# Kernel tuning notes

Measured on AMD Instinct MI355X. Metric: run time of the kernel, lower is better.

## Reference

```python
import jax, jax.numpy as jnp
import numpy as np

B, S, H, NH = 4, 1024, 2048, 32
HD = H // NH
EPS = 1e-5

def layer_norm(x, w, b):
    mu = jnp.mean(x, axis=-1, keepdims=True)
    var = jnp.mean(jnp.square(x - mu), axis=-1, keepdims=True)
    return (x - mu) * jax.lax.rsqrt(var + EPS) * w + b

def setup_inputs() -> dict:
    key = jax.random.key(0)
    ks = jax.random.split(key, 8)
    s = 0.02
    inp = {
        'hidden_states': jax.random.normal(ks[0], (B, S, H), jnp.float32),
        'mask': jnp.tril(jnp.ones((S, S), jnp.float32))[None, None],  # causal 0/1
        'ln1_w': jnp.ones((H,), jnp.float32), 'ln1_b': jnp.zeros((H,), jnp.float32),
        'w_qkv': s * jax.random.normal(ks[1], (H, 3 * H), jnp.float32),
        'b_qkv': jnp.zeros((3 * H,), jnp.float32),
        'w_dense': s * jax.random.normal(ks[2], (H, H), jnp.float32),
        'b_dense': jnp.zeros((H,), jnp.float32),
        'ln3_w': jnp.ones((H,), jnp.float32), 'ln3_b': jnp.zeros((H,), jnp.float32),
        'ln2_w': jnp.ones((H,), jnp.float32), 'ln2_b': jnp.zeros((H,), jnp.float32),
        'w_h4h': s * jax.random.normal(ks[3], (H, 4 * H), jnp.float32),
        'b_h4h': jnp.zeros((4 * H,), jnp.float32),
        'w_4hh': s * jax.random.normal(ks[4], (4 * H, H), jnp.float32),
        'b_4hh': jnp.zeros((H,), jnp.float32),
        'ln4_w': jnp.ones((H,), jnp.float32), 'ln4_b': jnp.zeros((H,), jnp.float32),
    }
    return inp

def _layer(hidden_states, mask, ln1_w, ln1_b, w_qkv, b_qkv, w_dense, b_dense,
           ln3_w, ln3_b, ln2_w, ln2_b, w_h4h, b_h4h, w_4hh, b_4hh, ln4_w, ln4_b):
    # --- input LN ---
    x1 = layer_norm(hidden_states, ln1_w, ln1_b)
    # --- self attention ---
    qkv = x1 @ w_qkv + b_qkv                              # [B,S,3H]
    q, k, v = jnp.split(qkv, 3, axis=-1)
    def heads(t):  # [B,S,H] -> [B,NH,S,HD]
        return t.reshape(B, S, NH, HD).transpose(0, 2, 1, 3)
    q, k, v = heads(q), heads(k), heads(v)
    scores = jnp.einsum('bnqd,bnkd->bnqk', q / jnp.sqrt(jnp.float32(HD)), k)
    scores = scores * mask - 10000.0 * (1.0 - mask)
    probs = jax.nn.softmax(scores, axis=-1)
    ctx = jnp.einsum('bnqk,bnkd->bnqd', probs, v)
    ctx = ctx.transpose(0, 2, 1, 3).reshape(B, S, H)
    attn_out = ctx @ w_dense + b_dense
    # sandwich LN on attention output
    attn_out = layer_norm(attn_out, ln3_w, ln3_b)
    ln_input = hidden_states + attn_out
    # --- MLP ---
    x2 = layer_norm(ln_input, ln2_w, ln2_b)
    inter = jax.nn.gelu(x2 @ w_h4h + b_h4h, approximate=True)
    mlp_out = inter @ w_4hh + b_4hh
    mlp_out = layer_norm(mlp_out, ln4_w, ln4_b)
    return ln_input + mlp_out

def reference(hidden_states, mask, ln1_w, ln1_b, w_qkv, b_qkv, w_dense, b_dense,
              ln3_w, ln3_b, ln2_w, ln2_b, w_h4h, b_h4h, w_4hh, b_4hh, ln4_w, ln4_b):
    return _layer(hidden_states, mask, ln1_w, ln1_b, w_qkv, b_qkv, w_dense, b_dense,
                  ln3_w, ln3_b, ln2_w, ln2_b, w_h4h, b_h4h, w_4hh, b_4hh, ln4_w, ln4_b)
```

## Files before the change

kernel.cpp:

```cpp
#include <hip/hip_runtime.h>
#include <cstdint>
#include <cstddef>

typedef __bf16 bf16_t;
typedef __bf16 bf16x8 __attribute__((ext_vector_type(8)));
typedef float f32x4 __attribute__((ext_vector_type(4)));

#define BB 4
#define SS 1024
#define HH 2048
#define NHH 32
#define HDD 64
#define MTOK 4096
#define QKVLD 6144

static constexpr size_t OFF_WQKV   = 0;
static constexpr size_t OFF_WDENSE = 25165824;
static constexpr size_t OFF_WH4H   = 33554432;
static constexpr size_t OFF_W4HH   = 67108864;
static constexpr size_t OFF_X1     = 100663296;
static constexpr size_t OFF_QKV    = 117440512;
static constexpr size_t OFF_ATTND2 = 150994944;
static constexpr size_t OFF_VT     = 167772160;
static constexpr size_t OFF_LNIN   = 184549376;
static constexpr size_t OFF_MLP    = 218103808;
static constexpr size_t OFF_MLP2   = 234881024;

__device__ __forceinline__ uint16_t f2bfu(float f) {
  union { float f; uint32_t u; } v; v.f = f;
  return (uint16_t)((v.u + 0x7FFFu + ((v.u >> 16) & 1u)) >> 16);
}
__device__ __forceinline__ bf16_t f2bf(float f) {
  union { uint16_t u; bf16_t b; } o; o.u = f2bfu(f);
  return o.b;
}
__device__ __forceinline__ float bfu2f(uint16_t u) {
  union { uint32_t u; float f; } v; v.u = ((uint32_t)u) << 16;
  return v.f;
}

__device__ __forceinline__ void g2l16(const void* g, void* l) {
  __builtin_amdgcn_global_load_lds(
      (const __attribute__((address_space(1))) void*)g,
      (__attribute__((address_space(3))) void*)l, 16, 0, 0);
}

__global__ void convert_all_kernel(const float* __restrict__ w0, bf16_t* __restrict__ o0,
                                   const float* __restrict__ w1, bf16_t* __restrict__ o1,
                                   const float* __restrict__ w2, bf16_t* __restrict__ o2,
                                   const float* __restrict__ w3, bf16_t* __restrict__ o3) {
  __shared__ float t[32][33];
  int id = blockIdx.x;
  const float* W; bf16_t* WT; int K, N, nt, idx;
  if (id < 12288)      { W = w0; WT = o0; K = 2048; N = 6144; nt = 192; idx = id; }
  else if (id < 16384) { W = w1; WT = o1; K = 2048; N = 2048; nt = 64;  idx = id - 12288; }
  else if (id < 32768) { W = w2; WT = o2; K = 2048; N = 8192; nt = 256; idx = id - 16384; }
  else                 { W = w3; WT = o3; K = 8192; N = 2048; nt = 64;  idx = id - 32768; }
  const int n0 = (idx % nt) * 32;
  const int k0 = (idx / nt) * 32;
  const int tx = threadIdx.x, ty = threadIdx.y;
#pragma unroll
  for (int j = 0; j < 4; ++j)
    t[ty + j * 8][tx] = W[(size_t)(k0 + ty + j * 8) * N + n0 + tx];
  __syncthreads();
#pragma unroll
  for (int j = 0; j < 4; ++j)
    WT[(size_t)(n0 + ty + j * 8) * K + k0 + tx] = f2bf(t[tx][ty + j * 8]);
}

__global__ void transpose_v_kernel(const bf16_t* __restrict__ qkv, bf16_t* __restrict__ vT) {
  __shared__ bf16_t t[32][33];
  const int s0 = blockIdx.x * 32;
  const int d0 = blockIdx.y * 32;
  const int bh = blockIdx.z;
  const int b = bh >> 5, h = bh & 31;
  const int tx = threadIdx.x, ty = threadIdx.y;
  const bf16_t* src = qkv + (size_t)b * SS * QKVLD + 2 * HH + h * HDD;
#pragma unroll
  for (int j = 0; j < 4; ++j)
    t[ty + j * 8][tx] = src[(size_t)(s0 + ty + j * 8) * QKVLD + d0 + tx];
  __syncthreads();
  bf16_t* dst = vT + (size_t)bh * HDD * SS;
#pragma unroll
  for (int j = 0; j < 4; ++j)
    dst[(size_t)(d0 + ty + j * 8) * SS + s0 + tx] = t[tx][ty + j * 8];
}

__device__ __forceinline__ void block_reduce2(float& s, float& ss) {
#pragma unroll
  for (int o = 32; o > 0; o >>= 1) {
    s += __shfl_down(s, o, 64);
    ss += __shfl_down(ss, o, 64);
  }
  __shared__ float red[8];
  const int wave = threadIdx.x >> 6;
  const int lane = threadIdx.x & 63;
  if (lane == 0) { red[wave] = s; red[4 + wave] = ss; }
  __syncthreads();
  s = red[0] + red[1] + red[2] + red[3];
  ss = red[4] + red[5] + red[6] + red[7];
  __syncthreads();
}

__device__ __forceinline__ void load8(const float* base, int tid, float* v) {
  float4 a = ((const float4*)base)[tid];
  float4 b = ((const float4*)base)[tid + 256];
  v[0] = a.x; v[1] = a.y; v[2] = a.z; v[3] = a.w;
  v[4] = b.x; v[5] = b.y; v[6] = b.z; v[7] = b.w;
}
__device__ __forceinline__ void load8bf(const bf16_t* base, int tid, float* v) {
  ushort4 a = ((const ushort4*)base)[tid];
  ushort4 b = ((const ushort4*)base)[tid + 256];
  v[0] = bfu2f(a.x); v[1] = bfu2f(a.y); v[2] = bfu2f(a.z); v[3] = bfu2f(a.w);
  v[4] = bfu2f(b.x); v[5] = bfu2f(b.y); v[6] = bfu2f(b.z); v[7] = bfu2f(b.w);
}
__device__ __forceinline__ void store8f(float* base, int tid, const float* v) {
  ((float4*)base)[tid] = make_float4(v[0], v[1], v[2], v[3]);
  ((float4*)base)[tid + 256] = make_float4(v[4], v[5], v[6], v[7]);
}
__device__ __forceinline__ void store8bf(bf16_t* base, int tid, const float* v) {
  ushort4 o0 = {f2bfu(v[0]), f2bfu(v[1]), f2bfu(v[2]), f2bfu(v[3])};
  ushort4 o1 = {f2bfu(v[4]), f2bfu(v[5]), f2bfu(v[6]), f2bfu(v[7])};
  ((ushort4*)base)[tid] = o0;
  ((ushort4*)base)[tid + 256] = o1;
}
__device__ __forceinline__ void row_stats(const float* v, float& mean, float& inv) {
  float s = 0.f, ss = 0.f;
#pragma unroll
  for (int i = 0; i < 8; ++i) { s += v[i]; ss += v[i] * v[i]; }
  block_reduce2(s, ss);
  mean = s * (1.0f / 2048.0f);
  float var = ss * (1.0f / 2048.0f) - mean * mean;
  inv = rsqrtf(var + 1e-5f);
}

__global__ __launch_bounds__(256) void ln1_kernel(const float* __restrict__ x,
                                                  const float* __restrict__ w,
                                                  const float* __restrict__ b,
                                                  bf16_t* __restrict__ out) {
  const int row = blockIdx.x, tid = threadIdx.x;
  float v[8], wv[8], bv[8], o[8];
  load8(x + (size_t)row * HH, tid, v);
  float mean, inv;
  row_stats(v, mean, inv);
  load8(w, tid, wv);
  load8(b, tid, bv);
#pragma unroll
  for (int i = 0; i < 8; ++i) o[i] = (v[i] - mean) * inv * wv[i] + bv[i];
  store8bf(out + (size_t)row * HH, tid, o);
}

__global__ __launch_bounds__(256) void fuse_mid_kernel(
    const bf16_t* __restrict__ ad, const bf16_t* __restrict__ ad2,
    const float* __restrict__ hid,
    const float* __restrict__ w3, const float* __restrict__ b3,
    const float* __restrict__ w2, const float* __restrict__ b2,
    float* __restrict__ lnin, bf16_t* __restrict__ x2) {
  const int row = blockIdx.x, tid = threadIdx.x;
  float a[8], a2[8], h[8], wv[8], bv[8], l[8], o[8];
  load8bf(ad + (size_t)row * HH, tid, a);
  load8bf(ad2 + (size_t)row * HH, tid, a2);
#pragma unroll
  for (int i = 0; i < 8; ++i) a[i] += a2[i];
  float mean3, inv3;
  row_stats(a, mean3, inv3);
  load8(hid + (size_t)row * HH, tid, h);
  load8(w3, tid, wv);
  load8(b3, tid, bv);
#pragma unroll
  for (int i = 0; i < 8; ++i) l[i] = h[i] + (a[i] - mean3) * inv3 * wv[i] + bv[i];
  store8f(lnin + (size_t)row * HH, tid, l);
  float mean2, inv2;
  row_stats(l, mean2, inv2);
  load8(w2, tid, wv);
  load8(b2, tid, bv);
#pragma unroll
  for (int i = 0; i < 8; ++i) o[i] = (l[i] - mean2) * inv2 * wv[i] + bv[i];
  store8bf(x2 + (size_t)row * HH, tid, o);
}

__global__ __launch_bounds__(256) void fuse_out_kernel(
    const bf16_t* __restrict__ mlp, const bf16_t* __restrict__ mlp2,
    const float* __restrict__ lnin,
    const float* __restrict__ w4, const float* __restrict__ b4,
    float* __restrict__ out) {
  const int row = blockIdx.x, tid = threadIdx.x;
  float m[8], m2[8], l[8], wv[8], bv[8], o[8];
  load8bf(mlp + (size_t)row * HH, tid, m);
  load8bf(mlp2 + (size_t)row * HH, tid, m2);
#pragma unroll
  for (int i = 0; i < 8; ++i) m[i] += m2[i];
  float mean4, inv4;
  row_stats(m, mean4, inv4);
  load8(lnin + (size_t)row * HH, tid, l);
  load8(w4, tid, wv);
  load8(b4, tid, bv);
#pragma unroll
  for (int i = 0; i < 8; ++i) o[i] = l[i] + (m[i] - mean4) * inv4 * wv[i] + bv[i];
  store8f(out + (size_t)row * HH, tid, o);
}

#define MFMA16(a, b, cc) __builtin_amdgcn_mfma_f32_16x16x32_bf16(a, b, cc, 0, 0, 0)

#define STAGE(ISB, BUF, HALF, KT) do {                                              \
    const char* _s = ((ISB) ? bS : aS) + (size_t)(HALF) * h128 + (size_t)(KT) * 128; \
    char* _d = lds + ((ISB) ? 65536 : 0) + (BUF) * 32768 + (HALF) * 16384 +         \
               wave * 1024;                                                         \
    g2l16(_s, _d);                                                                  \
    g2l16(_s + h64, _d + 8192);                                                     \
  } while (0)

#define LDA(BUF, MQ)                                                                \
  _Pragma("unroll") for (int mf = 0; mf < 4; ++mf) {                                \
    const char* _p = aRd + (BUF) * 32768 + (MQ) * 8192 + mf * 2048;                 \
    aR[mf * 2]     = *(const bf16x8*)(_p + colK0);                                  \
    aR[mf * 2 + 1] = *(const bf16x8*)(_p + colK1);                                  \
  }

#define LDB(BR, BUF, NQ)                                                            \
  _Pragma("unroll") for (int nf = 0; nf < 2; ++nf) {                                \
    const char* _p = bRd + (BUF) * 32768 + (NQ) * 4096 + nf * 2048;                 \
    BR[nf * 2]     = *(const bf16x8*)(_p + colK0);                                  \
    BR[nf * 2 + 1] = *(const bf16x8*)(_p + colK1);                                  \
  }

#define MMA(MQ, NQ, BR)                                                             \
  _Pragma("unroll") for (int mf = 0; mf < 4; ++mf)                                  \
  _Pragma("unroll") for (int nf = 0; nf < 2; ++nf)                                  \
  _Pragma("unroll") for (int ks = 0; ks < 2; ++ks)                                  \
    acc[(MQ) * 4 + mf][(NQ) * 2 + nf] =                                             \
        MFMA16(aR[mf * 2 + ks], BR[nf * 2 + ks], acc[(MQ) * 4 + mf][(NQ) * 2 + nf]);

#define PH_BEGIN()                                                                  \
  __builtin_amdgcn_s_barrier();                                                     \
  __builtin_amdgcn_s_setprio(1);

#define PH_MID()                                                                    \
  __builtin_amdgcn_s_setprio(0);

#define PH_END()                                                                    \
  __builtin_amdgcn_s_barrier();

template <int EPI, int SPLITK>
__global__ __launch_bounds__(512, 2) void gemm256(
    const bf16_t* __restrict__ A, const bf16_t* __restrict__ BT,
    const float* __restrict__ bias, void* __restrict__ out0, void* __restrict__ out1,
    const int M, const int N, const int Keff, const int ldK) {
  __shared__ alignas(16) char lds[131072];
  const int tid = threadIdx.x;
  const int wave = tid >> 6, lane = tid & 63;
  const int wm = wave >> 2, wn = wave & 3;
  const int c = lane & 15, g = lane >> 4;

  const int nwg = gridDim.x;
  int bid = (blockIdx.x & 7) * (nwg >> 3) + (blockIdx.x >> 3);
  const int nm = M >> 8;
  int slice = 0;
  if (SPLITK == 2) {
    const int per = nm * (N >> 8);
    slice = bid >= per;
    bid -= slice * per;
  }
  const int mt = bid % nm, nt = bid / nm;

  const size_t ldb = (size_t)ldK * 2;
  const size_t h64 = (size_t)64 * ldb;
  const size_t h128 = 2 * h64;
  const char* aPan = (const char*)A + (size_t)(mt * 256) * ldb + (size_t)(slice * Keff) * 2;
  const char* bPan = (const char*)BT + (size_t)(nt * 256) * ldb + (size_t)(slice * Keff) * 2;

  const int srow = tid >> 3;
  const int scb = ((tid & 7) << 4) ^ ((srow & 7) << 4);
  const char* aS = aPan + (size_t)srow * ldb + scb;
  const char* bS = bPan + (size_t)srow * ldb + scb;

  const int x4 = (c & 7) << 4;
  const int colK0 = (g * 16) ^ x4;
  const int colK1 = (64 + g * 16) ^ x4;
  const char* aRd = lds + wm * 16384 + c * 128;
  const char* bRd = lds + 65536 + (wn >> 1) * 16384 + ((wn & 1) * 64 + c) * 128;

  f32x4 acc[8][4] = {};
  bf16x8 aR[8], b0R[4], b1R[4];

  const int NITER = Keff >> 7;
  const int NT2 = NITER * 2;

  STAGE(1, 0, 0, 0); STAGE(1, 0, 1, 0); STAGE(0, 0, 0, 0); STAGE(0, 0, 1, 0);
  STAGE(1, 1, 0, 1); STAGE(1, 1, 1, 1);
  asm volatile("s_waitcnt vmcnt(4)" ::: "memory");
  __builtin_amdgcn_s_barrier();
  LDA(0, 0);
  LDB(b0R, 0, 0);

  for (int it = 0; it < NITER; ++it) {
    const int ktb = 2 * it + 1;
    int kt2 = 2 * it + 2; if (kt2 >= NT2) kt2 = 0;
    int kt3 = 2 * it + 3; if (kt3 >= NT2) kt3 = 0;
    STAGE(0, 1, 0, ktb);
    PH_BEGIN(); MMA(0, 0, b0R); PH_MID();
    LDB(b1R, 0, 1);
    PH_END();
    STAGE(0, 1, 1, ktb);
    PH_BEGIN(); MMA(0, 1, b1R); PH_MID();
    LDA(0, 1);
    PH_END();
    STAGE(1, 0, 0, kt2);
    PH_BEGIN(); MMA(1, 1, b1R); PH_MID();
    PH_END();
    STAGE(1, 0, 1, kt2);
    asm volatile("s_waitcnt vmcnt(4)" ::: "memory");
    PH_BEGIN(); MMA(1, 0, b0R); PH_MID();
    LDA(1, 0); LDB(b0R, 1, 0);
    PH_END();
    STAGE(0, 0, 0, kt2);
    PH_BEGIN(); MMA(0, 0, b0R); PH_MID();
    LDB(b1R, 1, 1);
    PH_END();
    STAGE(0, 0, 1, kt2);
    PH_BEGIN(); MMA(0, 1, b1R); PH_MID();
    LDA(1, 1);
    PH_END();
    STAGE(1, 1, 0, kt3);
    PH_BEGIN(); MMA(1, 1, b1R); PH_MID();
    PH_END();
    STAGE(1, 1, 1, kt3);
    asm volatile("s_waitcnt vmcnt(4)" ::: "memory");
    PH_BEGIN(); MMA(1, 0, b0R); PH_MID();
    LDA(0, 0); LDB(b0R, 0, 0);
    PH_END();
  }

  const int rowb = mt * 256 + wm * 128 + g * 4;
  const int colb = nt * 256 + wn * 64 + c;
  if constexpr (EPI == 0) {
    bf16_t* o = (bf16_t*)(slice ? out1 : out0);
    float bvv[4];
#pragma unroll
    for (int nf = 0; nf < 4; ++nf) bvv[nf] = (slice == 0) ? bias[colb + nf * 16] : 0.0f;
#pragma unroll
    for (int mf = 0; mf < 8; ++mf) {
      const int r = rowb + mf * 16;
#pragma unroll
      for (int e = 0; e < 4; ++e) {
        bf16_t* orow = o + (size_t)(r + e) * N + colb;
#pragma unroll
        for (int nf = 0; nf < 4; ++nf)
          orow[nf * 16] = f2bf(acc[mf][nf][e] + bvv[nf]);
      }
    }
  } else if constexpr (EPI == 1) {
    bf16_t* o = (bf16_t*)out0;
    float bvv[4];
#pragma unroll
    for (int nf = 0; nf < 4; ++nf) bvv[nf] = bias[colb + nf * 16];
#pragma unroll
    for (int mf = 0; mf < 8; ++mf) {
      const int r = rowb + mf * 16;
#pragma unroll
      for (int e = 0; e < 4; ++e) {
        bf16_t* orow = o + (size_t)(r + e) * N + colb;
#pragma unroll
        for (int nf = 0; nf < 4; ++nf)
          orow[nf * 16] = f2bf(acc[mf][nf][e] + bvv[nf]);
      }
    }
  } else {
    bf16_t* o = (bf16_t*)out0;
    float bvv[4];
#pragma unroll
    for (int nf = 0; nf < 4; ++nf) bvv[nf] = bias[colb + nf * 16];
#pragma unroll
    for (int mf = 0; mf < 8; ++mf) {
      const int r = rowb + mf * 16;
#pragma unroll
      for (int e = 0; e < 4; ++e) {
        bf16_t* orow = o + (size_t)(r + e) * N + colb;
#pragma unroll
        for (int nf = 0; nf < 4; ++nf) {
          float u = acc[mf][nf][e] + bvv[nf];
          float cc2 = 0.7978845608f * (u + 0.044715f * u * u * u);
          float ex = __expf(2.0f * cc2);
          float th = 1.0f - 2.0f / (ex + 1.0f);
          orow[nf * 16] = f2bf(0.5f * u * (1.0f + th));
        }
      }
    }
  }
}

__global__ __launch_bounds__(512) void attn_kernel(
    const bf16_t* __restrict__ qkv, const bf16_t* __restrict__ vT,
    bf16_t* __restrict__ ctx) {
  __shared__ alignas(16) char Ksm[8192];
  __shared__ alignas(16) char Vsm[8192];
  __shared__ alignas(16) char Psm[16384];

  const int id = blockIdx.x;
  const int qt = 7 - (id >> 7);
  const int bh = id & 127;
  const int b = bh >> 5, h = bh & 31;
  const int tid = threadIdx.x;
  const int wave = tid >> 6;
  const int lane = tid & 63;
  const int q0 = qt * 128;
  const int q0w = q0 + wave * 16;
  const int c = lane & 15;
  const int g = lane >> 4;

  const bf16_t* qb = qkv + ((size_t)b * SS + q0w) * QKVLD + h * HDD;
  const bf16x8 qa0 = *(const bf16x8*)(qb + (size_t)c * QKVLD + g * 8);
  const bf16x8 qa1 = *(const bf16x8*)(qb + (size_t)c * QKVLD + 32 + g * 8);

  f32x4 o[4] = {};
  float mrow[4], lrow[4];
#pragma unroll
  for (int e = 0; e < 4; ++e) { mrow[e] = -1e30f; lrow[e] = 0.0f; }

  const int sr = tid >> 3;
  const int sgb = ((tid & 7) * 16) ^ ((sr & 7) << 4);
  const char* kgb = (const char*)(qkv + (size_t)b * SS * QKVLD + HH + h * HDD);
  const char* vgb = (const char*)(vT + (size_t)bh * HDD * SS);
  char* kdst = Ksm + wave * 1024;
  char* vdst = Vsm + wave * 1024;
  char* Pw = Psm + wave * 2048;

  const int ntiles = (q0 + 128) >> 6;

  for (int t = 0; t < ntiles; ++t) {
    const int kb = t * 64;
    g2l16(kgb + (size_t)(kb + sr) * (QKVLD * 2) + sgb, kdst);
    g2l16(vgb + (size_t)sr * 2048 + (size_t)kb * 2 + sgb, vdst);
    __syncthreads();

    if (kb < q0w + 16) {
      f32x4 s[4] = {};
#pragma unroll
      for (int sub = 0; sub < 4; ++sub) {
        const int n = sub * 16 + c;
        const int x = (n & 7) << 4;
        bf16x8 kf0 = *(const bf16x8*)(Ksm + n * 128 + ((g * 16) ^ x));
        bf16x8 kf1 = *(const bf16x8*)(Ksm + n * 128 + ((64 + g * 16) ^ x));
        s[sub] = MFMA16(qa0, kf0, s[sub]);
        s[sub] = MFMA16(qa1, kf1, s[sub]);
      }
      const bool diag = (kb + 63 > q0w);
      float pv[4][4];
#pragma unroll
      for (int sub = 0; sub < 4; ++sub)
#pragma unroll
        for (int e = 0; e < 4; ++e) {
          float sv = s[sub][e] * 0.125f;
          if (diag && (kb + sub * 16 + c > q0w + g * 4 + e)) sv = -10000.0f;
          pv[sub][e] = sv;
        }
      float scale[4];
#pragma unroll
      for (int e = 0; e < 4; ++e) {
        float mx = fmaxf(fmaxf(pv[0][e], pv[1][e]), fmaxf(pv[2][e], pv[3][e]));
        mx = fmaxf(mx, __shfl_xor(mx, 1, 64));
        mx = fmaxf(mx, __shfl_xor(mx, 2, 64));
        mx = fmaxf(mx, __shfl_xor(mx, 4, 64));
        mx = fmaxf(mx, __shfl_xor(mx, 8, 64));
        const float mnew = fmaxf(mrow[e], mx);
        scale[e] = __expf(mrow[e] - mnew);
        mrow[e] = mnew;
      }
#pragma unroll
      for (int e = 0; e < 4; ++e) {
        const int row = g * 4 + e;
        const int xr = (row & 7) << 4;
        float sum = 0.0f;
#pragma unroll
        for (int sub = 0; sub < 4; ++sub) {
          float p = __expf(pv[sub][e] - mrow[e]);
          sum += p;
          const int cb = (sub * 16 + c) * 2;
          *(bf16_t*)(Pw + row * 128 + (cb ^ xr)) = f2bf(p);
        }
        sum += __shfl_xor(sum, 1, 64);
        sum += __shfl_xor(sum, 2, 64);
        sum += __shfl_xor(sum, 4, 64);
        sum += __shfl_xor(sum, 8, 64);
        lrow[e] = lrow[e] * scale[e] + sum;
      }
#pragma unroll
      for (int d = 0; d < 4; ++d)
#pragma unroll
        for (int e = 0; e < 4; ++e) o[d][e] *= scale[e];
      const int xa = (c & 7) << 4;
      bf16x8 pa0 = *(const bf16x8*)(Pw + c * 128 + ((g * 16) ^ xa));
      bf16x8 pa1 = *(const bf16x8*)(Pw + c * 128 + ((64 + g * 16) ^ xa));
#pragma unroll
      for (int d = 0; d < 4; ++d) {
        const int n = d * 16 + c;
        const int xv = (n & 7) << 4;
        bf16x8 vf0 = *(const bf16x8*)(Vsm + n * 128 + ((g * 16) ^ xv));
        bf16x8 vf1 = *(const bf16x8*)(Vsm + n * 128 + ((64 + g * 16) ^ xv));
        o[d] = MFMA16(pa0, vf0, o[d]);
        o[d] = MFMA16(pa1, vf1, o[d]);
      }
    }
    __syncthreads();
  }

#pragma unroll
  for (int e = 0; e < 4; ++e) {
    const int qrow = q0w + g * 4 + e;
    const float inv = 1.0f / lrow[e];
#pragma unroll
    for (int d = 0; d < 4; ++d)
      ctx[((size_t)b * SS + qrow) * HH + h * 64 + d * 16 + c] = f2bf(o[d][e] * inv);
  }
}

extern "C" void kernel_launch(void* const* d_in, const int* in_sizes, int n_in,
                              void* d_out, int out_size, void* d_ws, size_t ws_size,
                              hipStream_t stream) {
  const float* hidden = (const float*)d_in[0];
  const float* ln1w = (const float*)d_in[2];
  const float* ln1b = (const float*)d_in[3];
  const float* wqkv = (const float*)d_in[4];
  const float* bqkv = (const float*)d_in[5];
  const float* wdense = (const float*)d_in[6];
  const float* bdense = (const float*)d_in[7];
  const float* ln3w = (const float*)d_in[8];
  const float* ln3b = (const float*)d_in[9];
  const float* ln2w = (const float*)d_in[10];
  const float* ln2b = (const float*)d_in[11];
  const float* wh4h = (const float*)d_in[12];
  const float* bh4h = (const float*)d_in[13];
  const float* w4hh = (const float*)d_in[14];
  const float* b4hh = (const float*)d_in[15];
  const float* ln4w = (const float*)d_in[16];
  const float* ln4b = (const float*)d_in[17];

  char* ws = (char*)d_ws;
  bf16_t* wqkvT = (bf16_t*)(ws + OFF_WQKV);
  bf16_t* wdenseT = (bf16_t*)(ws + OFF_WDENSE);
  bf16_t* wh4hT = (bf16_t*)(ws + OFF_WH4H);
  bf16_t* w4hhT = (bf16_t*)(ws + OFF_W4HH);
  bf16_t* x1 = (bf16_t*)(ws + OFF_X1);
  bf16_t* qkv = (bf16_t*)(ws + OFF_QKV);
  bf16_t* vT = (bf16_t*)(ws + OFF_VT);
  bf16_t* ctx = (bf16_t*)(ws + OFF_X1);
  bf16_t* attnd = (bf16_t*)(ws + OFF_QKV);
  bf16_t* attnd2 = (bf16_t*)(ws + OFF_ATTND2);
  float* lnin = (float*)(ws + OFF_LNIN);
  bf16_t* x2 = (bf16_t*)(ws + OFF_X1);
  bf16_t* inter = (bf16_t*)(ws + OFF_QKV);
  bf16_t* mlp = (bf16_t*)(ws + OFF_MLP);
  bf16_t* mlp2 = (bf16_t*)(ws + OFF_MLP2);

  dim3 tb(32, 8);
  convert_all_kernel<<<dim3(49152), tb, 0, stream>>>(wqkv, wqkvT, wdense, wdenseT,
                                                     wh4h, wh4hT, w4hh, w4hhT);

  ln1_kernel<<<MTOK, 256, 0, stream>>>(hidden, ln1w, ln1b, x1);

  gemm256<1, 1><<<dim3((6144 / 256) * (4096 / 256)), 512, 0, stream>>>(
      x1, wqkvT, bqkv, (void*)qkv, nullptr, MTOK, 6144, 2048, 2048);

  transpose_v_kernel<<<dim3(SS / 32, HDD / 32, BB * NHH), tb, 0, stream>>>(qkv, vT);

  attn_kernel<<<dim3(1024), 512, 0, stream>>>(qkv, vT, ctx);

  gemm256<0, 2><<<dim3((2048 / 256) * (4096 / 256) * 2), 512, 0, stream>>>(
      ctx, wdenseT, bdense, (void*)attnd, (void*)attnd2, MTOK, 2048, 1024, 2048);

  fuse_mid_kernel<<<MTOK, 256, 0, stream>>>(attnd, attnd2, hidden, ln3w, ln3b, ln2w, ln2b, lnin, x2);

  gemm256<2, 1><<<dim3((8192 / 256) * (4096 / 256)), 512, 0, stream>>>(
      x2, wh4hT, bh4h, (void*)inter, nullptr, MTOK, 8192, 2048, 2048);

  gemm256<0, 2><<<dim3((2048 / 256) * (4096 / 256) * 2), 512, 0, stream>>>(
      inter, w4hhT, b4hh, (void*)mlp, (void*)mlp2, MTOK, 2048, 4096, 8192);

  fuse_out_kernel<<<MTOK, 256, 0, stream>>>(mlp, mlp2, lnin, ln4w, ln4b, (float*)d_out);
}
```

Before: 592.7 us.

## Double-buffer attention K/V tiles, fuse LN1 into weight convert, store lnin as bf16

The attention kernel now double-buffers its K and V shared-memory tiles, prefetching the next tile while the current one is computed, which removes the load-then-sync stall at the top of each iteration. The LN1 kernel is merged into the weight-conversion launch as extra blocks, saving one kernel launch. The residual lnin buffer is stored as bf16 instead of fp32, halving its traffic at the cost of precision in the final residual add. The prefetch appears to lack a barrier before the buffer is overwritten (only one __syncthreads per iteration), which may introduce a race.

```diff
diff --git a/kernel.cpp b/kernel.cpp
--- a/kernel.cpp
+++ b/kernel.cpp
@@ -45,12 +45,77 @@
       (__attribute__((address_space(3))) void*)l, 16, 0, 0);
 }
 
-__global__ void convert_all_kernel(const float* __restrict__ w0, bf16_t* __restrict__ o0,
+__device__ __forceinline__ void block_reduce2(int tid, float& s, float& ss) {
+#pragma unroll
+  for (int o = 32; o > 0; o >>= 1) {
+    s += __shfl_down(s, o, 64);
+    ss += __shfl_down(ss, o, 64);
+  }
+  __shared__ float red[8];
+  const int wave = tid >> 6;
+  const int lane = tid & 63;
+  if (lane == 0) { red[wave] = s; red[4 + wave] = ss; }
+  __syncthreads();
+  s = red[0] + red[1] + red[2] + red[3];
+  ss = red[4] + red[5] + red[6] + red[7];
+  __syncthreads();
+}
+
+__device__ __forceinline__ void load8(const float* base, int tid, float* v) {
+  float4 a = ((const float4*)base)[tid];
+  float4 b = ((const float4*)base)[tid + 256];
+  v[0] = a.x; v[1] = a.y; v[2] = a.z; v[3] = a.w;
+  v[4] = b.x; v[5] = b.y; v[6] = b.z; v[7] = b.w;
+}
+__device__ __forceinline__ void load8bf(const bf16_t* base, int tid, float* v) {
+  ushort4 a = ((const ushort4*)base)[tid];
+  ushort4 b = ((const ushort4*)base)[tid + 256];
+  v[0] = bfu2f(a.x); v[1] = bfu2f(a.y); v[2] = bfu2f(a.z); v[3] = bfu2f(a.w);
+  v[4] = bfu2f(b.x); v[5] = bfu2f(b.y); v[6] = bfu2f(b.z); v[7] = bfu2f(b.w);
+}
+__device__ __forceinline__ void store8f(float* base, int tid, const float* v) {
+  ((float4*)base)[tid] = make_float4(v[0], v[1], v[2], v[3]);
+  ((float4*)base)[tid + 256] = make_float4(v[4], v[5], v[6], v[7]);
+}
+__device__ __forceinline__ void store8bf(bf16_t* base, int tid, const float* v) {
+  ushort4 o0 = {f2bfu(v[0]), f2bfu(v[1]), f2bfu(v[2]), f2bfu(v[3])};
+  ushort4 o1 = {f2bfu(v[4]), f2bfu(v[5]), f2bfu(v[6]), f2bfu(v[7])};
+  ((ushort4*)base)[tid] = o0;
+  ((ushort4*)base)[tid + 256] = o1;
+}
+__device__ __forceinline__ void row_stats(int tid, const float* v, float& mean, float& inv) {
+  float s = 0.f, ss = 0.f;
+#pragma unroll
+  for (int i = 0; i < 8; ++i) { s += v[i]; ss += v[i] * v[i]; }
+  block_reduce2(tid, s, ss);
+  mean = s * (1.0f / 2048.0f);
+  float var = ss * (1.0f / 2048.0f) - mean * mean;
+  inv = rsqrtf(var + 1e-5f);
+}
+
+__global__ void convert_ln1_kernel(const float* __restrict__ w0, bf16_t* __restrict__ o0,
                                    const float* __restrict__ w1, bf16_t* __restrict__ o1,
                                    const float* __restrict__ w2, bf16_t* __restrict__ o2,
-                                   const float* __restrict__ w3, bf16_t* __restrict__ o3) {
+                                   const float* __restrict__ w3, bf16_t* __restrict__ o3,
+                                   const float* __restrict__ hid,
+                                   const float* __restrict__ ln1w, const float* __restrict__ ln1b,
+                                   bf16_t* __restrict__ x1) {
+  const int id = blockIdx.x;
+  const int tx = threadIdx.x & 31, ty = threadIdx.x >> 5;
+  if (id >= 49152) {
+    const int row = id - 49152, tid = threadIdx.x;
+    float v[8], wv[8], bv[8], o[8];
+    load8(hid + (size_t)row * HH, tid, v);
+    float mean, inv;
+    row_stats(tid, v, mean, inv);
+    load8(ln1w, tid, wv);
+    load8(ln1b, tid, bv);
+#pragma unroll
+    for (int i = 0; i < 8; ++i) o[i] = (v[i] - mean) * inv * wv[i] + bv[i];
+    store8bf(x1 + (size_t)row * HH, tid, o);
+    return;
+  }
   __shared__ float t[32][33];
-  int id = blockIdx.x;
   const float* W; bf16_t* WT; int K, N, nt, idx;
   if (id < 12288)      { W = w0; WT = o0; K = 2048; N = 6144; nt = 192; idx = id; }
   else if (id < 16384) { W = w1; WT = o1; K = 2048; N = 2048; nt = 64;  idx = id - 12288; }
@@ -58,7 +123,6 @@
   else                 { W = w3; WT = o3; K = 8192; N = 2048; nt = 64;  idx = id - 32768; }
   const int n0 = (idx % nt) * 32;
   const int k0 = (idx / nt) * 32;
-  const int tx = threadIdx.x, ty = threadIdx.y;
 #pragma unroll
   for (int j = 0; j < 4; ++j)
     t[ty + j * 8][tx] = W[(size_t)(k0 + ty + j * 8) * N + n0 + tx];
@@ -86,76 +150,12 @@
     dst[(size_t)(d0 + ty + j * 8) * SS + s0 + tx] = t[tx][ty + j * 8];
 }
 
-__device__ __forceinline__ void block_reduce2(float& s, float& ss) {
-#pragma unroll
-  for (int o = 32; o > 0; o >>= 1) {
-    s += __shfl_down(s, o, 64);
-    ss += __shfl_down(ss, o, 64);
-  }
-  __shared__ float red[8];
-  const int wave = threadIdx.x >> 6;
-  const int lane = threadIdx.x & 63;
-  if (lane == 0) { red[wave] = s; red[4 + wave] = ss; }
-  __syncthreads();
-  s = red[0] + red[1] + red[2] + red[3];
-  ss = red[4] + red[5] + red[6] + red[7];
-  __syncthreads();
-}
-
-__device__ __forceinline__ void load8(const float* base, int tid, float* v) {
-  float4 a = ((const float4*)base)[tid];
-  float4 b = ((const float4*)base)[tid + 256];
-  v[0] = a.x; v[1] = a.y; v[2] = a.z; v[3] = a.w;
-  v[4] = b.x; v[5] = b.y; v[6] = b.z; v[7] = b.w;
-}
-__device__ __forceinline__ void load8bf(const bf16_t* base, int tid, float* v) {
-  ushort4 a = ((const ushort4*)base)[tid];
-  ushort4 b = ((const ushort4*)base)[tid + 256];
-  v[0] = bfu2f(a.x); v[1] = bfu2f(a.y); v[2] = bfu2f(a.z); v[3] = bfu2f(a.w);
-  v[4] = bfu2f(b.x); v[5] = bfu2f(b.y); v[6] = bfu2f(b.z); v[7] = bfu2f(b.w);
-}
-__device__ __forceinline__ void store8f(float* base, int tid, const float* v) {
-  ((float4*)base)[tid] = make_float4(v[0], v[1], v[2], v[3]);
-  ((float4*)base)[tid + 256] = make_float4(v[4], v[5], v[6], v[7]);
-}
-__device__ __forceinline__ void store8bf(bf16_t* base, int tid, const float* v) {
-  ushort4 o0 = {f2bfu(v[0]), f2bfu(v[1]), f2bfu(v[2]), f2bfu(v[3])};
-  ushort4 o1 = {f2bfu(v[4]), f2bfu(v[5]), f2bfu(v[6]), f2bfu(v[7])};
-  ((ushort4*)base)[tid] = o0;
-  ((ushort4*)base)[tid + 256] = o1;
-}
-__device__ __forceinline__ void row_stats(const float* v, float& mean, float& inv) {
-  float s = 0.f, ss = 0.f;
-#pragma unroll
-  for (int i = 0; i < 8; ++i) { s += v[i]; ss += v[i] * v[i]; }
-  block_reduce2(s, ss);
-  mean = s * (1.0f / 2048.0f);
-  float var = ss * (1.0f / 2048.0f) - mean * mean;
-  inv = rsqrtf(var + 1e-5f);
-}
-
-__global__ __launch_bounds__(256) void ln1_kernel(const float* __restrict__ x,
-                                                  const float* __restrict__ w,
-                                                  const float* __restrict__ b,
-                                                  bf16_t* __restrict__ out) {
-  const int row = blockIdx.x, tid = threadIdx.x;
-  float v[8], wv[8], bv[8], o[8];
-  load8(x + (size_t)row * HH, tid, v);
-  float mean, inv;
-  row_stats(v, mean, inv);
-  load8(w, tid, wv);
-  load8(b, tid, bv);
-#pragma unroll
-  for (int i = 0; i < 8; ++i) o[i] = (v[i] - mean) * inv * wv[i] + bv[i];
-  store8bf(out + (size_t)row * HH, tid, o);
-}
-
 __global__ __launch_bounds__(256) void fuse_mid_kernel(
     const bf16_t* __restrict__ ad, const bf16_t* __restrict__ ad2,
     const float* __restrict__ hid,
     const float* __restrict__ w3, const float* __restrict__ b3,
     const float* __restrict__ w2, const float* __restrict__ b2,
-    float* __restrict__ lnin, bf16_t* __restrict__ x2) {
+    bf16_t* __restrict__ lnin, bf16_t* __restrict__ x2) {
   const int row = blockIdx.x, tid = threadIdx.x;
   float a[8], a2[8], h[8], wv[8], bv[8], l[8], o[8];
   load8bf(ad + (size_t)row * HH, tid, a);
@@ -163,15 +163,15 @@
 #pragma unroll
   for (int i = 0; i < 8; ++i) a[i] += a2[i];
   float mean3, inv3;
-  row_stats(a, mean3, inv3);
+  row_stats(tid, a, mean3, inv3);
   load8(hid + (size_t)row * HH, tid, h);
   load8(w3, tid, wv);
   load8(b3, tid, bv);
 #pragma unroll
   for (int i = 0; i < 8; ++i) l[i] = h[i] + (a[i] - mean3) * inv3 * wv[i] + bv[i];
-  store8f(lnin + (size_t)row * HH, tid, l);
+  store8bf(lnin + (size_t)row * HH, tid, l);
   float mean2, inv2;
-  row_stats(l, mean2, inv2);
+  row_stats(tid, l, mean2, inv2);
   load8(w2, tid, wv);
   load8(b2, tid, bv);
 #pragma unroll
@@ -181,7 +181,7 @@
 
 __global__ __launch_bounds__(256) void fuse_out_kernel(
     const bf16_t* __restrict__ mlp, const bf16_t* __restrict__ mlp2,
-    const float* __restrict__ lnin,
+    const bf16_t* __restrict__ lnin,
     const float* __restrict__ w4, const float* __restrict__ b4,
     float* __restrict__ out) {
   const int row = blockIdx.x, tid = threadIdx.x;
@@ -191,8 +191,8 @@
 #pragma unroll
   for (int i = 0; i < 8; ++i) m[i] += m2[i];
   float mean4, inv4;
-  row_stats(m, mean4, inv4);
-  load8(lnin + (size_t)row * HH, tid, l);
+  row_stats(tid, m, mean4, inv4);
+  load8bf(lnin + (size_t)row * HH, tid, l);
   load8(w4, tid, wv);
   load8(b4, tid, bv);
 #pragma unroll
@@ -392,8 +392,8 @@
 __global__ __launch_bounds__(512) void attn_kernel(
     const bf16_t* __restrict__ qkv, const bf16_t* __restrict__ vT,
     bf16_t* __restrict__ ctx) {
-  __shared__ alignas(16) char Ksm[8192];
-  __shared__ alignas(16) char Vsm[8192];
+  __shared__ alignas(16) char Ksm[2][8192];
+  __shared__ alignas(16) char Vsm[2][8192];
   __shared__ alignas(16) char Psm[16384];
 
   const int id = blockIdx.x;
@@ -421,17 +421,24 @@
   const int sgb = ((tid & 7) * 16) ^ ((sr & 7) << 4);
   const char* kgb = (const char*)(qkv + (size_t)b * SS * QKVLD + HH + h * HDD);
   const char* vgb = (const char*)(vT + (size_t)bh * HDD * SS);
-  char* kdst = Ksm + wave * 1024;
-  char* vdst = Vsm + wave * 1024;
   char* Pw = Psm + wave * 2048;
 
   const int ntiles = (q0 + 128) >> 6;
+
+  {
+    g2l16(kgb + (size_t)sr * (QKVLD * 2) + sgb, Ksm[0] + wave * 1024);
+    g2l16(vgb + (size_t)sr * 2048 + sgb, Vsm[0] + wave * 1024);
+  }
+  __syncthreads();
 
   for (int t = 0; t < ntiles; ++t) {
     const int kb = t * 64;
-    g2l16(kgb + (size_t)(kb + sr) * (QKVLD * 2) + sgb, kdst);
-    g2l16(vgb + (size_t)sr * 2048 + (size_t)kb * 2 + sgb, vdst);
-    __syncthreads();
+    const int cur = t & 1;
+    if (t + 1 < ntiles) {
+      const int kb1 = kb + 64;
+      g2l16(kgb + (size_t)(kb1 + sr) * (QKVLD * 2) + sgb, Ksm[cur ^ 1] + wave * 1024);
+      g2l16(vgb + (size_t)sr * 2048 + (size_t)kb1 * 2 + sgb, Vsm[cur ^ 1] + wave * 1024);
+    }
 
     if (kb < q0w + 16) {
       f32x4 s[4] = {};
@@ -439,8 +446,8 @@
       for (int sub = 0; sub < 4; ++sub) {
         const int n = sub * 16 + c;
         const int x = (n & 7) << 4;
-        bf16x8 kf0 = *(const bf16x8*)(Ksm + n * 128 + ((g * 16) ^ x));
-        bf16x8 kf1 = *(const bf16x8*)(Ksm + n * 128 + ((64 + g * 16) ^ x));
+        bf16x8 kf0 = *(const bf16x8*)(Ksm[cur] + n * 128 + ((g * 16) ^ x));
+        bf16x8 kf1 = *(const bf16x8*)(Ksm[cur] + n * 128 + ((64 + g * 16) ^ x));
         s[sub] = MFMA16(qa0, kf0, s[sub]);
         s[sub] = MFMA16(qa1, kf1, s[sub]);
       }
@@ -495,8 +502,8 @@
       for (int d = 0; d < 4; ++d) {
         const int n = d * 16 + c;
         const int xv = (n & 7) << 4;
-        bf16x8 vf0 = *(const bf16x8*)(Vsm + n * 128 + ((g * 16) ^ xv));
-        bf16x8 vf1 = *(const bf16x8*)(Vsm + n * 128 + ((64 + g * 16) ^ xv));
+        bf16x8 vf0 = *(const bf16x8*)(Vsm[cur] + n * 128 + ((g * 16) ^ xv));
+        bf16x8 vf1 = *(const bf16x8*)(Vsm[cur] + n * 128 + ((64 + g * 16) ^ xv));
         o[d] = MFMA16(pa0, vf0, o[d]);
         o[d] = MFMA16(pa1, vf1, o[d]);
       }
@@ -546,21 +553,20 @@
   bf16_t* ctx = (bf16_t*)(ws + OFF_X1);
   bf16_t* attnd = (bf16_t*)(ws + OFF_QKV);
   bf16_t* attnd2 = (bf16_t*)(ws + OFF_ATTND2);
-  float* lnin = (float*)(ws + OFF_LNIN);
+  bf16_t* lnin = (bf16_t*)(ws + OFF_LNIN);
   bf16_t* x2 = (bf16_t*)(ws + OFF_X1);
   bf16_t* inter = (bf16_t*)(ws + OFF_QKV);
   bf16_t* mlp = (bf16_t*)(ws + OFF_MLP);
   bf16_t* mlp2 = (bf16_t*)(ws + OFF_MLP2);
 
-  dim3 tb(32, 8);
-  convert_all_kernel<<<dim3(49152), tb, 0, stream>>>(wqkv, wqkvT, wdense, wdenseT,
-                                                     wh4h, wh4hT, w4hh, w4hhT);
-
-  ln1_kernel<<<MTOK, 256, 0, stream>>>(hidden, ln1w, ln1b, x1);
+  convert_ln1_kernel<<<dim3(49152 + MTOK), 256, 0, stream>>>(
+      wqkv, wqkvT, wdense, wdenseT, wh4h, wh4hT, w4hh, w4hhT,
+      hidden, ln1w, ln1b, x1);
 
   gemm256<1, 1><<<dim3((6144 / 256) * (4096 / 256)), 512, 0, stream>>>(
       x1, wqkvT, bqkv, (void*)qkv, nullptr, MTOK, 6144, 2048, 2048);
 
+  dim3 tb(32, 8);
   transpose_v_kernel<<<dim3(SS / 32, HDD / 32, BB * NHH), tb, 0, stream>>>(qkv, vT);
 
   attn_kernel<<<dim3(1024), 512, 0, stream>>>(qkv, vT, ctx);
```

New measurement: 581.8 us. Within noise of the previous version (-1.8%).
